# Performance work log

Hardware: AMD Instinct MI355X
Metric: run time of the kernel (lower is better)

The kernel has to match this reference:

```python
import jax, jax.numpy as jnp
import numpy as np

N, C, H, W = 8, 80, 100, 152          # batch, fg classes, stride-8 feature map of 800x1216 image
STRIDE = 8
P = H * W                              # points in this level
PRE_NMS_THRESH = 0.05                  # cfg.post.INFERENCE_TH
PRE_NMS_TOP_N = 1000                   # cfg.post.PRE_NMS_TOP_N
NMS_THRESH = 0.6                       # cfg.post.NMS_TH
POST_NMS_TOP_N = 100                   # cfg.post.DETECTIONS_PER_IMG
MIN_SIZE = 0.0
CLASS_OFFSET = 1.0e5                   # per-class NMS via coordinate-offset trick


def setup_inputs():
    key = jax.random.key(0)
    k1, k2, k3 = jax.random.split(key, 3)
    ys, xs = jnp.meshgrid(jnp.arange(H), jnp.arange(W), indexing='ij')
    locations = (jnp.stack([xs.reshape(-1), ys.reshape(-1)], axis=1).astype(jnp.float32) * STRIDE + STRIDE // 2)
    box_cls = jax.random.normal(k1, (N, C, H, W), jnp.float32) - 2.0
    box_regression = jax.random.uniform(k2, (N, 4, H, W), jnp.float32) * 64.0
    centerness = jax.random.normal(k3, (N, 1, H, W), jnp.float32)
    im_info = jnp.tile(jnp.array([[H * STRIDE, W * STRIDE]], jnp.float32), (N, 1))
    return {'locations': locations, 'box_cls': box_cls, 'box_regression': box_regression,
            'centerness': centerness, 'im_info': im_info}


def _iou_matrix(boxes):
    # boxes: [K, 4] (x1, y1, x2, y2)
    area = jnp.clip(boxes[:, 2] - boxes[:, 0], 0) * jnp.clip(boxes[:, 3] - boxes[:, 1], 0)
    lt = jnp.maximum(boxes[:, None, :2], boxes[None, :, :2])
    rb = jnp.minimum(boxes[:, None, 2:], boxes[None, :, 2:])
    wh = jnp.clip(rb - lt, 0)
    inter = wh[..., 0] * wh[..., 1]
    return inter / (area[:, None] + area[None, :] - inter + 1e-9)


def _single_image(locations, cls_logits, reg, ctr_logits, info):
    # [C,H,W] -> [P,C] matches permute(0,2,3,1).reshape(-1,C)
    cls = jax.nn.sigmoid(cls_logits.reshape(C, P).T)
    ctr = jax.nn.sigmoid(ctr_logits.reshape(P))
    cand = cls > PRE_NMS_THRESH
    scores = cls * ctr[:, None]
    flat = jnp.where(cand, scores, 0.0).reshape(-1)          # [P*C], zeros = non-candidates
    topv, topi = jax.lax.top_k(flat, PRE_NMS_TOP_N)          # pre-NMS top-n (sorted desc)
    loc = topi // C
    label = topi % C + 1
    valid = topv > 0.0
    r = reg.reshape(4, P).T[loc]                             # [K, 4] (l, t, r, b)
    pt = locations[loc]                                      # [K, 2]
    h_im, w_im = info[0], info[1]
    x1 = jnp.clip(pt[:, 0] - r[:, 0], 0.0, w_im - 1.0)
    y1 = jnp.clip(pt[:, 1] - r[:, 1], 0.0, h_im - 1.0)
    x2 = jnp.clip(pt[:, 0] + r[:, 2], 0.0, w_im - 1.0)
    y2 = jnp.clip(pt[:, 1] + r[:, 3], 0.0, h_im - 1.0)
    boxes = jnp.stack([x1, y1, x2, y2], axis=1)
    valid = valid & (x2 - x1 >= MIN_SIZE) & (y2 - y1 >= MIN_SIZE)  # remove_small_boxes
    sc = jnp.where(valid, topv, 0.0)
    # offset boxes by class so cross-class IoU is 0 -> equivalent to per-class NMS
    ob = boxes + (label.astype(boxes.dtype) * CLASS_OFFSET)[:, None]
    iou = _iou_matrix(ob)
    idx = jnp.arange(PRE_NMS_TOP_N)
    def body(i, keep):
        alive = keep[i] & valid[i]
        sup = alive & (iou[i] > NMS_THRESH) & (idx > i)
        return keep & ~sup
    keep = jax.lax.fori_loop(0, PRE_NMS_TOP_N, body, valid)  # greedy NMS (score-sorted)
    final_sc = jnp.where(keep, sc, 0.0)
    fv, fi = jax.lax.top_k(final_sc, POST_NMS_TOP_N)         # detections-per-image cap
    out = jnp.concatenate([boxes[fi], label[fi][:, None].astype(boxes.dtype), fv[:, None]], axis=1)
    return jnp.where((fv > 0.0)[:, None], out, 0.0)          # [POST_NMS_TOP_N, 6]


def reference(locations, box_cls, box_regression, centerness, im_info):
    # -> [N, POST_NMS_TOP_N, 6] = (x1, y1, x2, y2, label, score), zero-padded rows invalid
    return jax.vmap(lambda c, r, t, i: _single_image(locations, c, r, t, i))(
        box_cls, box_regression, centerness, im_info)
```

## Files before the change

### kernel.cpp

```cpp
#include <hip/hip_runtime.h>
#include <stdint.h>

#define NIMG 8
#define NCLS 80
#define HF 100
#define WF 152
#define NPTS (HF*WF)
#define NPC (NPTS*NCLS)
#define NF4 (NPC/4)
#define TOPK 1000
#define NSH 8
#define SHCAP 512
#define SORTN 4096
#define LBUF 1024
#define POSTK 100
#define HBLK 297
#define RBLK (SORTN/256)

static constexpr size_t B_H1    = 0;
static constexpr size_t B_CNT   = B_H1 + (size_t)NIMG*4096*4;
static constexpr size_t B_META  = B_CNT + (size_t)NIMG*NSH*4;
static constexpr size_t B_BMAX  = B_META + NIMG*4*4;
static constexpr size_t B_SKEY  = (B_BMAX + (size_t)NIMG*HBLK*4 + 7) & ~(size_t)7;
static constexpr size_t B_ZEND  = B_SKEY + (size_t)NIMG*1024*8;
static constexpr size_t B_CTRS  = (B_ZEND + 15) & ~(size_t)15;
static constexpr size_t B_CAND  = (B_CTRS + (size_t)NIMG*NPTS*4 + 15) & ~(size_t)15;
static constexpr size_t B_BOX   = B_CAND + (size_t)NIMG*NSH*SHCAP*8;
static constexpr size_t B_OBOX  = B_BOX + (size_t)NIMG*TOPK*16;
static constexpr size_t B_SC    = B_OBOX + (size_t)NIMG*TOPK*16;
static constexpr size_t B_VAL   = B_SC + (size_t)NIMG*TOPK*4;
static constexpr size_t B_LAB   = B_VAL + (size_t)NIMG*TOPK*4;
static constexpr size_t B_KEEP  = B_LAB + (size_t)NIMG*TOPK*4;

__device__ __forceinline__ float sigm(float x){ return 1.0f / (1.0f + expf(-x)); }

__global__ void __launch_bounds__(256)
k_ctrsig(const float* __restrict__ ctr, float* __restrict__ ctr_sig){
  int i4 = blockIdx.x * 256 + threadIdx.x;
  if (i4 < NIMG*NPTS/4){
    float4 v = ((const float4*)ctr)[i4];
    float4 o;
    o.x = sigm(v.x); o.y = sigm(v.y); o.z = sigm(v.z); o.w = sigm(v.w);
    ((float4*)ctr_sig)[i4] = o;
  }
}

__global__ void __launch_bounds__(256)
k_hist(const float* __restrict__ box_cls, const float* __restrict__ ctr_sig,
       uint32_t* __restrict__ h1, uint32_t* __restrict__ bmax){
  __shared__ uint32_t h[4096];
  __shared__ uint32_t smax;
  for (int i = threadIdx.x; i < 4096; i += 256) h[i] = 0;
  if (threadIdx.x == 0) smax = 0;
  __syncthreads();
  const int n = blockIdx.y;
  const float4* cls4 = (const float4*)(box_cls + (size_t)n * NPC);
  const float* cs = ctr_sig + (size_t)n * NPTS;
  const int base4 = blockIdx.x * 1024 + threadIdx.x;
  float4 a[4], b[4];
  bool ok[4];
  #pragma unroll
  for (int k = 0; k < 4; ++k){
    int i4 = base4 + k * 256;
    ok[k] = (i4 < NF4);
    if (ok[k]){
      a[k] = cls4[i4];
      uint32_t p0 = ((uint32_t)(i4 << 2)) % (uint32_t)NPTS;
      b[k] = *(const float4*)(cs + p0);
    }
  }
  __builtin_amdgcn_sched_barrier(0);
  uint32_t vmax = 0;
  #pragma unroll
  for (int k = 0; k < 4; ++k){
    if (!ok[k]) continue;
    float sv[4] = {a[k].x, a[k].y, a[k].z, a[k].w};
    float cv[4] = {b[k].x, b[k].y, b[k].z, b[k].w};
    #pragma unroll
    for (int j = 0; j < 4; ++j){
      float s = sigm(sv[j]);
      if (s > 0.05f){
        float sc = s * cv[j];
        if (sc > 0.0f){
          uint32_t bin = __float_as_uint(sc) >> 18;
          atomicAdd(&h[bin], 1u);
          vmax = (bin > vmax) ? bin : vmax;
        }
      }
    }
  }
  if (vmax) atomicMax(&smax, vmax);
  __syncthreads();
  uint32_t* g = h1 + (size_t)n * 4096;
  for (int i = threadIdx.x; i < 4096; i += 256){
    uint32_t v = h[i];
    if (v) atomicAdd(&g[i], v);
  }
  if (threadIdx.x == 0) bmax[n * HBLK + blockIdx.x] = smax;
}

__global__ void k_scan(const uint32_t* __restrict__ h1, uint32_t* __restrict__ meta){
  const int n = blockIdx.x;
  const uint32_t* h = h1 + (size_t)n * 4096;
  __shared__ uint32_t psum[256];
  __shared__ uint32_t suff[256];
  const int t = threadIdx.x;
  uint32_t s = 0;
  #pragma unroll
  for (int i = 0; i < 16; ++i) s += h[t * 16 + i];
  psum[t] = s;
  __syncthreads();
  if (t == 0){
    uint32_t acc = 0;
    for (int seg = 255; seg >= 0; --seg){ suff[seg] = acc; acc += psum[seg]; }
  }
  __syncthreads();
  if (suff[t] < TOPK && suff[t] + psum[t] >= TOPK){
    uint32_t acc = suff[t];
    for (int b = t * 16 + 15; b >= t * 16; --b){
      uint32_t hb = h[b];
      if (acc + hb >= TOPK){
        meta[n * 4 + 0] = acc;
        meta[n * 4 + 1] = (uint32_t)b;
        break;
      }
      acc += hb;
    }
  }
}

__global__ void __launch_bounds__(256)
k_collect(const float* __restrict__ box_cls, const float* __restrict__ ctr_sig,
          const uint32_t* __restrict__ meta, const uint32_t* __restrict__ bmax,
          uint32_t* __restrict__ cnt, uint64_t* __restrict__ cand){
  __shared__ uint64_t buf[LBUF];
  __shared__ uint32_t lcnt;
  __shared__ uint32_t gbase;
  const int n = blockIdx.y;
  const uint32_t T = meta[n * 4 + 1];
  if (bmax[n * HBLK + blockIdx.x] < T) return;
  if (threadIdx.x == 0) lcnt = 0;
  __syncthreads();
  const float4* cls4 = (const float4*)(box_cls + (size_t)n * NPC);
  const float* cs = ctr_sig + (size_t)n * NPTS;
  const int base4 = blockIdx.x * 1024 + threadIdx.x;
  float4 a[4], b[4];
  int p0a[4], ca[4];
  bool ok[4];
  #pragma unroll
  for (int k = 0; k < 4; ++k){
    int i4 = base4 + k * 256;
    ok[k] = (i4 < NF4);
    if (ok[k]){
      a[k] = cls4[i4];
      uint32_t e0 = (uint32_t)(i4 << 2);
      uint32_t c = e0 / (uint32_t)NPTS;
      uint32_t p0 = e0 - c * (uint32_t)NPTS;
      ca[k] = (int)c; p0a[k] = (int)p0;
      b[k] = *(const float4*)(cs + p0);
    }
  }
  __builtin_amdgcn_sched_barrier(0);
  #pragma unroll
  for (int k = 0; k < 4; ++k){
    if (!ok[k]) continue;
    float sv[4] = {a[k].x, a[k].y, a[k].z, a[k].w};
    float cv[4] = {b[k].x, b[k].y, b[k].z, b[k].w};
    #pragma unroll
    for (int j = 0; j < 4; ++j){
      float s = sigm(sv[j]);
      if (s > 0.05f){
        float sc = s * cv[j];
        if (sc > 0.0f){
          uint32_t bits = __float_as_uint(sc);
          if ((bits >> 18) >= T){
            uint32_t f = (uint32_t)(p0a[k] + j) * NCLS + (uint32_t)ca[k];
            uint32_t pos = atomicAdd(&lcnt, 1u);
            if (pos < LBUF)
              buf[pos] = ((uint64_t)bits << 32) | (uint64_t)(0xFFFFFFFFu - f);
          }
        }
      }
    }
  }
  __syncthreads();
  uint32_t c = lcnt; if (c > LBUF) c = LBUF;
  const int sh = blockIdx.x & (NSH - 1);
  if (threadIdx.x == 0 && c) gbase = atomicAdd(&cnt[n * NSH + sh], c);
  __syncthreads();
  for (uint32_t i = threadIdx.x; i < c; i += 256){
    uint32_t p = gbase + i;
    if (p < SHCAP) cand[(((size_t)n * NSH + sh) << 9) + p] = buf[i];
  }
}

__global__ void __launch_bounds__(256)
k_rank(const uint32_t* __restrict__ cnt, const uint64_t* __restrict__ cand,
       uint64_t* __restrict__ skey){
  __shared__ alignas(16) uint64_t keys[SORTN + 4];
  __shared__ uint32_t cs_s[NSH], pre_s[NSH + 1];
  const int n = blockIdx.y;
  const int t = threadIdx.x;
  if (t == 0){
    uint32_t acc = 0;
    for (int s = 0; s < NSH; ++s){
      uint32_t c = cnt[n * NSH + s]; if (c > SHCAP) c = SHCAP;
      cs_s[s] = c; pre_s[s] = acc; acc += c;
    }
    pre_s[NSH] = acc;
  }
  __syncthreads();
  const int total = (int)pre_s[NSH];
  const int base = blockIdx.x * 256;
  if (base >= total) return;
  for (int i = t; i < SORTN; i += 256){
    int s = i >> 9, j = i & (SHCAP - 1);
    if ((uint32_t)j < cs_s[s])
      keys[pre_s[s] + j] = cand[(((size_t)n * NSH + s) << 9) + j];
  }
  if (t < 4) keys[total + t] = 0ull;
  __syncthreads();
  const int g = base + t;
  const uint64_t my = (g < total) ? keys[g] : 0ull;
  uint32_t rank = 0;
  const int tot4 = (total + 3) & ~3;
  for (int i = 0; i < tot4; i += 4){
    rank += (keys[i]     > my) ? 1u : 0u;
    rank += (keys[i + 1] > my) ? 1u : 0u;
    rank += (keys[i + 2] > my) ? 1u : 0u;
    rank += (keys[i + 3] > my) ? 1u : 0u;
  }
  if (g < total && rank < TOPK)
    skey[(size_t)n * 1024 + rank] = my;
}

__global__ void __launch_bounds__(1024)
k_decode(const uint64_t* __restrict__ skey,
         const float* __restrict__ locations, const float* __restrict__ box_reg,
         const float* __restrict__ im_info,
         float* __restrict__ boxw, float* __restrict__ oboxw, float* __restrict__ scw,
         uint32_t* __restrict__ valw, uint32_t* __restrict__ labw){
  const int n = blockIdx.x;
  const int t = threadIdx.x;
  if (t < TOPK){
    uint64_t kk = skey[(size_t)n * 1024 + t];
    uint32_t bits = (uint32_t)(kk >> 32);
    uint32_t fi = 0xFFFFFFFFu - (uint32_t)(kk & 0xFFFFFFFFull);
    float v = __uint_as_float(bits);
    int loc = 0, ci = 0;
    if (v > 0.0f){ loc = (int)(fi / NCLS); ci = (int)(fi - (uint32_t)loc * NCLS); }
    float px = locations[2 * loc], py = locations[2 * loc + 1];
    const float* rg = box_reg + (size_t)n * 4 * NPTS;
    float rl = rg[loc], rt = rg[NPTS + loc], rr = rg[2 * NPTS + loc], rb = rg[3 * NPTS + loc];
    float h_im = im_info[n * 2 + 0], w_im = im_info[n * 2 + 1];
    float x1 = fminf(fmaxf(px - rl, 0.0f), w_im - 1.0f);
    float y1 = fminf(fmaxf(py - rt, 0.0f), h_im - 1.0f);
    float x2 = fminf(fmaxf(px + rr, 0.0f), w_im - 1.0f);
    float y2 = fminf(fmaxf(py + rb, 0.0f), h_im - 1.0f);
    bool valid = (v > 0.0f) && (__fsub_rn(x2, x1) >= 0.0f) && (__fsub_rn(y2, y1) >= 0.0f);
    float scv = valid ? v : 0.0f;
    float lab = (float)(ci + 1);
    float off = __fmul_rn(lab, 100000.0f);
    size_t b4 = ((size_t)n * TOPK + t) * 4;
    boxw[b4 + 0] = x1; boxw[b4 + 1] = y1; boxw[b4 + 2] = x2; boxw[b4 + 3] = y2;
    oboxw[b4 + 0] = __fadd_rn(x1, off); oboxw[b4 + 1] = __fadd_rn(y1, off);
    oboxw[b4 + 2] = __fadd_rn(x2, off); oboxw[b4 + 3] = __fadd_rn(y2, off);
    size_t b1 = (size_t)n * TOPK + t;
    scw[b1] = scv; valw[b1] = valid ? 1u : 0u; labw[b1] = (uint32_t)(ci + 1);
  }
}

__global__ void __launch_bounds__(64)
k_nms(const uint32_t* __restrict__ labw, const float* __restrict__ oboxw,
      const uint32_t* __restrict__ valw, uint32_t* __restrict__ keepw){
  const int n = blockIdx.y;
  const int c = blockIdx.x;
  const int L = threadIdx.x;
  __shared__ uint16_t lst_s[TOPK];
  const uint32_t target = (uint32_t)(c + 1);
  uint32_t kcnt = 0;
  for (int i0 = 0; i0 < TOPK; i0 += 64){
    int slot = i0 + L;
    uint32_t lab = (slot < TOPK) ? labw[n * TOPK + slot] : 0u;
    bool m = (lab == target);
    uint64_t mask = __ballot(m);
    uint32_t pre = (uint32_t)__popcll(mask & ((1ull << L) - 1ull));
    if (m) lst_s[kcnt + pre] = (uint16_t)slot;
    kcnt += (uint32_t)__popcll(mask);
  }
  __syncthreads();
  if (kcnt == 0) return;
  if (kcnt <= 64){
    int gi = 0, kp = 0;
    float b0 = 0, b1 = 0, b2 = 0, b3 = 0, ar = 0;
    if (L < (int)kcnt){
      gi = (int)lst_s[L];
      size_t a4 = ((size_t)n * TOPK + gi) * 4;
      b0 = oboxw[a4 + 0]; b1 = oboxw[a4 + 1]; b2 = oboxw[a4 + 2]; b3 = oboxw[a4 + 3];
      kp = (valw[n * TOPK + gi] != 0) ? 1 : 0;
      ar = __fmul_rn(fmaxf(__fsub_rn(b2, b0), 0.0f), fmaxf(__fsub_rn(b3, b1), 0.0f));
    }
    for (int i = 0; i + 1 < (int)kcnt; ++i){
      int alive = __shfl(kp, i);
      float xi0 = __shfl(b0, i), xi1 = __shfl(b1, i), xi2 = __shfl(b2, i), xi3 = __shfl(b3, i);
      float ai = __shfl(ar, i);
      if (alive && L > i && kp){
        float ltx = fmaxf(xi0, b0), lty = fmaxf(xi1, b1);
        float rbx = fminf(xi2, b2), rby = fminf(xi3, b3);
        float w = fmaxf(__fsub_rn(rbx, ltx), 0.0f);
        float h = fmaxf(__fsub_rn(rby, lty), 0.0f);
        float inter = __fmul_rn(w, h);
        float den = __fadd_rn(__fsub_rn(__fadd_rn(ai, ar), inter), 1e-9f);
        if (inter / den > 0.6f) kp = 0;
      }
    }
    if (L < (int)kcnt) keepw[n * TOPK + gi] = (uint32_t)kp;
  } else if (L == 0){
    for (uint32_t i = 0; i < kcnt; ++i){
      int gi = (int)lst_s[i];
      keepw[n * TOPK + gi] = valw[n * TOPK + gi];
    }
    for (uint32_t i = 0; i < kcnt; ++i){
      int gi = (int)lst_s[i];
      if (!keepw[n * TOPK + gi]) continue;
      size_t a4 = ((size_t)n * TOPK + gi) * 4;
      float x0 = oboxw[a4], x1 = oboxw[a4 + 1], x2 = oboxw[a4 + 2], x3 = oboxw[a4 + 3];
      float ai = __fmul_rn(fmaxf(__fsub_rn(x2, x0), 0.0f), fmaxf(__fsub_rn(x3, x1), 0.0f));
      for (uint32_t j = i + 1; j < kcnt; ++j){
        int gj = (int)lst_s[j];
        if (!keepw[n * TOPK + gj]) continue;
        size_t c4 = ((size_t)n * TOPK + gj) * 4;
        float y0 = oboxw[c4], y1 = oboxw[c4 + 1], y2 = oboxw[c4 + 2], y3 = oboxw[c4 + 3];
        float aj = __fmul_rn(fmaxf(__fsub_rn(y2, y0), 0.0f), fmaxf(__fsub_rn(y3, y1), 0.0f));
        float ltx = fmaxf(x0, y0), lty = fmaxf(x1, y1);
        float rbx = fminf(x2, y2), rby = fminf(x3, y3);
        float w = fmaxf(__fsub_rn(rbx, ltx), 0.0f);
        float h = fmaxf(__fsub_rn(rby, lty), 0.0f);
        float inter = __fmul_rn(w, h);
        float den = __fadd_rn(__fsub_rn(__fadd_rn(ai, aj), inter), 1e-9f);
        if (inter / den > 0.6f) keepw[n * TOPK + gj] = 0;
      }
    }
  }
}

__global__ void __launch_bounds__(256)
k_final(const uint32_t* __restrict__ keepw, const float* __restrict__ boxw,
        const uint32_t* __restrict__ labw, const float* __restrict__ scw,
        float* __restrict__ out){
  const int n = blockIdx.x;
  __shared__ uint16_t fi_s[TOPK];
  __shared__ uint32_t wsum[4];
  const int t = threadIdx.x;
  const int i0 = t * 4;
  uint32_t f[4];
  #pragma unroll
  for (int j = 0; j < 4; ++j)
    f[j] = (i0 + j < TOPK) ? keepw[n * TOPK + i0 + j] : 0u;
  uint32_t lsum = f[0] + f[1] + f[2] + f[3];
  uint32_t sc = lsum;
  #pragma unroll
  for (int d = 1; d < 64; d <<= 1){
    uint32_t v = __shfl_up(sc, d);
    if ((t & 63) >= d) sc += v;
  }
  if ((t & 63) == 63) wsum[t >> 6] = sc;
  __syncthreads();
  uint32_t base = sc - lsum;
  for (int w = 0; w < (t >> 6); ++w) base += wsum[w];
  uint32_t p = base;
  #pragma unroll
  for (int j = 0; j < 4; ++j){
    if (f[j]){ if (p < TOPK) fi_s[p] = (uint16_t)(i0 + j); ++p; }
  }
  __syncthreads();
  uint32_t total = wsum[0] + wsum[1] + wsum[2] + wsum[3];
  if (t < POSTK){
    float* row = out + ((size_t)n * POSTK + t) * 6;
    if (t < (int)total){
      int i = (int)fi_s[t];
      size_t b4 = ((size_t)n * TOPK + i) * 4;
      row[0] = boxw[b4]; row[1] = boxw[b4 + 1]; row[2] = boxw[b4 + 2]; row[3] = boxw[b4 + 3];
      row[4] = (float)labw[n * TOPK + i]; row[5] = scw[n * TOPK + i];
    } else {
      row[0] = 0.0f; row[1] = 0.0f; row[2] = 0.0f;
      row[3] = 0.0f; row[4] = 0.0f; row[5] = 0.0f;
    }
  }
}

extern "C" void kernel_launch(void* const* d_in, const int* in_sizes, int n_in,
                              void* d_out, int out_size, void* d_ws, size_t ws_size,
                              hipStream_t stream){
  const float* locations = (const float*)d_in[0];
  const float* box_cls   = (const float*)d_in[1];
  const float* box_reg   = (const float*)d_in[2];
  const float* ctr       = (const float*)d_in[3];
  const float* im_info   = (const float*)d_in[4];
  float* out = (float*)d_out;
  char* ws = (char*)d_ws;
  uint32_t* h1    = (uint32_t*)(ws + B_H1);
  uint32_t* cnt   = (uint32_t*)(ws + B_CNT);
  uint32_t* meta  = (uint32_t*)(ws + B_META);
  uint32_t* bmax  = (uint32_t*)(ws + B_BMAX);
  uint64_t* skey  = (uint64_t*)(ws + B_SKEY);
  float*    ctrs  = (float*)(ws + B_CTRS);
  uint64_t* cand  = (uint64_t*)(ws + B_CAND);
  float*    boxw  = (float*)(ws + B_BOX);
  float*    oboxw = (float*)(ws + B_OBOX);
  float*    scw   = (float*)(ws + B_SC);
  uint32_t* valw  = (uint32_t*)(ws + B_VAL);
  uint32_t* labw  = (uint32_t*)(ws + B_LAB);
  uint32_t* keepw = (uint32_t*)(ws + B_KEEP);

  hipMemsetAsync(d_ws, 0, B_ZEND, stream);
  k_ctrsig<<<dim3((NIMG*NPTS/4 + 255)/256), 256, 0, stream>>>(ctr, ctrs);
  dim3 scang(HBLK, NIMG);
  k_hist<<<scang, 256, 0, stream>>>(box_cls, ctrs, h1, bmax);
  k_scan<<<NIMG, 256, 0, stream>>>(h1, meta);
  k_collect<<<scang, 256, 0, stream>>>(box_cls, ctrs, meta, bmax, cnt, cand);
  k_rank<<<dim3(RBLK, NIMG), 256, 0, stream>>>(cnt, cand, skey);
  k_decode<<<NIMG, 1024, 0, stream>>>(skey, locations, box_reg, im_info,
                                      boxw, oboxw, scw, valw, labw);
  k_nms<<<dim3(NCLS, NIMG), 64, 0, stream>>>(labw, oboxw, valw, keepw);
  k_final<<<NIMG, 256, 0, stream>>>(keepw, boxw, labw, scw, out);
}
```

Before: 190.5 us.

## Fuse decode, NMS and final compaction into one LDS-resident tail kernel

Merges the decode, per-class NMS and final compaction kernels into a single kernel per image. Boxes, scores, labels and keep flags stay in shared memory, and 16 wavefronts each handle a subset of classes. It also drops the workspace hipMemsetAsync by having the centerness-sigmoid kernel zero the histogram, counter and key buffers. The aim is to cut launch overhead and global round-trips. In exchange, per-class NMS runs on 16 waves per image instead of 80 independent blocks, so there is less parallelism in that phase.

```diff
diff --git a/kernel.cpp b/kernel.cpp
--- a/kernel.cpp
+++ b/kernel.cpp
@@ -16,33 +16,31 @@
 #define POSTK 100
 #define HBLK 297
 #define RBLK (SORTN/256)
-
-static constexpr size_t B_H1    = 0;
-static constexpr size_t B_CNT   = B_H1 + (size_t)NIMG*4096*4;
-static constexpr size_t B_META  = B_CNT + (size_t)NIMG*NSH*4;
-static constexpr size_t B_BMAX  = B_META + NIMG*4*4;
-static constexpr size_t B_SKEY  = (B_BMAX + (size_t)NIMG*HBLK*4 + 7) & ~(size_t)7;
-static constexpr size_t B_ZEND  = B_SKEY + (size_t)NIMG*1024*8;
-static constexpr size_t B_CTRS  = (B_ZEND + 15) & ~(size_t)15;
-static constexpr size_t B_CAND  = (B_CTRS + (size_t)NIMG*NPTS*4 + 15) & ~(size_t)15;
-static constexpr size_t B_BOX   = B_CAND + (size_t)NIMG*NSH*SHCAP*8;
-static constexpr size_t B_OBOX  = B_BOX + (size_t)NIMG*TOPK*16;
-static constexpr size_t B_SC    = B_OBOX + (size_t)NIMG*TOPK*16;
-static constexpr size_t B_VAL   = B_SC + (size_t)NIMG*TOPK*4;
-static constexpr size_t B_LAB   = B_VAL + (size_t)NIMG*TOPK*4;
-static constexpr size_t B_KEEP  = B_LAB + (size_t)NIMG*TOPK*4;
+#define ZWORDS (NIMG*4096 + NIMG*NSH + NIMG*4)
+
+static constexpr size_t B_H1   = 0;
+static constexpr size_t B_CNT  = B_H1 + (size_t)NIMG*4096*4;
+static constexpr size_t B_META = B_CNT + (size_t)NIMG*NSH*4;
+static constexpr size_t B_BMAX = B_META + NIMG*4*4;
+static constexpr size_t B_SKEY = (B_BMAX + (size_t)NIMG*HBLK*4 + 7) & ~(size_t)7;
+static constexpr size_t B_CTRS = (B_SKEY + (size_t)NIMG*1024*8 + 15) & ~(size_t)15;
+static constexpr size_t B_CAND = (B_CTRS + (size_t)NIMG*NPTS*4 + 15) & ~(size_t)15;
 
 __device__ __forceinline__ float sigm(float x){ return 1.0f / (1.0f + expf(-x)); }
 
 __global__ void __launch_bounds__(256)
-k_ctrsig(const float* __restrict__ ctr, float* __restrict__ ctr_sig){
-  int i4 = blockIdx.x * 256 + threadIdx.x;
-  if (i4 < NIMG*NPTS/4){
-    float4 v = ((const float4*)ctr)[i4];
+k_ctrsig(const float* __restrict__ ctr, float* __restrict__ ctr_sig,
+         uint32_t* __restrict__ zr, uint64_t* __restrict__ skey){
+  const int gid = blockIdx.x * 256 + threadIdx.x;
+  const int nthr = 119 * 256;
+  if (gid < NIMG*NPTS/4){
+    float4 v = ((const float4*)ctr)[gid];
     float4 o;
     o.x = sigm(v.x); o.y = sigm(v.y); o.z = sigm(v.z); o.w = sigm(v.w);
-    ((float4*)ctr_sig)[i4] = o;
-  }
+    ((float4*)ctr_sig)[gid] = o;
+  }
+  for (int i = gid; i < ZWORDS; i += nthr) zr[i] = 0u;
+  for (int i = gid; i < NIMG*1024; i += nthr) skey[i] = 0ull;
 }
 
 __global__ void __launch_bounds__(256)
@@ -235,20 +233,28 @@
 }
 
 __global__ void __launch_bounds__(1024)
-k_decode(const uint64_t* __restrict__ skey,
-         const float* __restrict__ locations, const float* __restrict__ box_reg,
-         const float* __restrict__ im_info,
-         float* __restrict__ boxw, float* __restrict__ oboxw, float* __restrict__ scw,
-         uint32_t* __restrict__ valw, uint32_t* __restrict__ labw){
+k_tail(const uint64_t* __restrict__ skey, const float* __restrict__ locations,
+       const float* __restrict__ box_reg, const float* __restrict__ im_info,
+       float* __restrict__ out){
+  __shared__ float bx[TOPK * 4];
+  __shared__ float ob[TOPK * 4];
+  __shared__ float scs[TOPK];
+  __shared__ alignas(4) uint8_t labs[TOPK];
+  __shared__ alignas(4) uint8_t keep[TOPK];
+  __shared__ uint16_t lst[16][64];
+  __shared__ uint16_t fi[POSTK];
+  __shared__ uint32_t wsum[16];
+  __shared__ uint32_t total_s;
   const int n = blockIdx.x;
   const int t = threadIdx.x;
+  const int w = t >> 6, lane = t & 63;
   if (t < TOPK){
     uint64_t kk = skey[(size_t)n * 1024 + t];
-    uint32_t bits = (uint32_t)(kk >> 32);
-    uint32_t fi = 0xFFFFFFFFu - (uint32_t)(kk & 0xFFFFFFFFull);
-    float v = __uint_as_float(bits);
+    uint32_t bitsv = (uint32_t)(kk >> 32);
+    uint32_t fidx = 0xFFFFFFFFu - (uint32_t)(kk & 0xFFFFFFFFull);
+    float v = __uint_as_float(bitsv);
     int loc = 0, ci = 0;
-    if (v > 0.0f){ loc = (int)(fi / NCLS); ci = (int)(fi - (uint32_t)loc * NCLS); }
+    if (v > 0.0f){ loc = (int)(fidx / NCLS); ci = (int)(fidx - (uint32_t)loc * NCLS); }
     float px = locations[2 * loc], py = locations[2 * loc + 1];
     const float* rg = box_reg + (size_t)n * 4 * NPTS;
     float rl = rg[loc], rt = rg[NPTS + loc], rr = rg[2 * NPTS + loc], rb = rg[3 * NPTS + loc];
@@ -258,130 +264,89 @@
     float x2 = fminf(fmaxf(px + rr, 0.0f), w_im - 1.0f);
     float y2 = fminf(fmaxf(py + rb, 0.0f), h_im - 1.0f);
     bool valid = (v > 0.0f) && (__fsub_rn(x2, x1) >= 0.0f) && (__fsub_rn(y2, y1) >= 0.0f);
-    float scv = valid ? v : 0.0f;
-    float lab = (float)(ci + 1);
-    float off = __fmul_rn(lab, 100000.0f);
-    size_t b4 = ((size_t)n * TOPK + t) * 4;
-    boxw[b4 + 0] = x1; boxw[b4 + 1] = y1; boxw[b4 + 2] = x2; boxw[b4 + 3] = y2;
-    oboxw[b4 + 0] = __fadd_rn(x1, off); oboxw[b4 + 1] = __fadd_rn(y1, off);
-    oboxw[b4 + 2] = __fadd_rn(x2, off); oboxw[b4 + 3] = __fadd_rn(y2, off);
-    size_t b1 = (size_t)n * TOPK + t;
-    scw[b1] = scv; valw[b1] = valid ? 1u : 0u; labw[b1] = (uint32_t)(ci + 1);
-  }
-}
-
-__global__ void __launch_bounds__(64)
-k_nms(const uint32_t* __restrict__ labw, const float* __restrict__ oboxw,
-      const uint32_t* __restrict__ valw, uint32_t* __restrict__ keepw){
-  const int n = blockIdx.y;
-  const int c = blockIdx.x;
-  const int L = threadIdx.x;
-  __shared__ uint16_t lst_s[TOPK];
-  const uint32_t target = (uint32_t)(c + 1);
-  uint32_t kcnt = 0;
-  for (int i0 = 0; i0 < TOPK; i0 += 64){
-    int slot = i0 + L;
-    uint32_t lab = (slot < TOPK) ? labw[n * TOPK + slot] : 0u;
-    bool m = (lab == target);
-    uint64_t mask = __ballot(m);
-    uint32_t pre = (uint32_t)__popcll(mask & ((1ull << L) - 1ull));
-    if (m) lst_s[kcnt + pre] = (uint16_t)slot;
-    kcnt += (uint32_t)__popcll(mask);
-  }
-  __syncthreads();
-  if (kcnt == 0) return;
-  if (kcnt <= 64){
-    int gi = 0, kp = 0;
-    float b0 = 0, b1 = 0, b2 = 0, b3 = 0, ar = 0;
-    if (L < (int)kcnt){
-      gi = (int)lst_s[L];
-      size_t a4 = ((size_t)n * TOPK + gi) * 4;
-      b0 = oboxw[a4 + 0]; b1 = oboxw[a4 + 1]; b2 = oboxw[a4 + 2]; b3 = oboxw[a4 + 3];
-      kp = (valw[n * TOPK + gi] != 0) ? 1 : 0;
-      ar = __fmul_rn(fmaxf(__fsub_rn(b2, b0), 0.0f), fmaxf(__fsub_rn(b3, b1), 0.0f));
-    }
-    for (int i = 0; i + 1 < (int)kcnt; ++i){
-      int alive = __shfl(kp, i);
-      float xi0 = __shfl(b0, i), xi1 = __shfl(b1, i), xi2 = __shfl(b2, i), xi3 = __shfl(b3, i);
-      float ai = __shfl(ar, i);
-      if (alive && L > i && kp){
-        float ltx = fmaxf(xi0, b0), lty = fmaxf(xi1, b1);
-        float rbx = fminf(xi2, b2), rby = fminf(xi3, b3);
-        float w = fmaxf(__fsub_rn(rbx, ltx), 0.0f);
-        float h = fmaxf(__fsub_rn(rby, lty), 0.0f);
-        float inter = __fmul_rn(w, h);
-        float den = __fadd_rn(__fsub_rn(__fadd_rn(ai, ar), inter), 1e-9f);
-        if (inter / den > 0.6f) kp = 0;
-      }
-    }
-    if (L < (int)kcnt) keepw[n * TOPK + gi] = (uint32_t)kp;
-  } else if (L == 0){
-    for (uint32_t i = 0; i < kcnt; ++i){
-      int gi = (int)lst_s[i];
-      keepw[n * TOPK + gi] = valw[n * TOPK + gi];
-    }
-    for (uint32_t i = 0; i < kcnt; ++i){
-      int gi = (int)lst_s[i];
-      if (!keepw[n * TOPK + gi]) continue;
-      size_t a4 = ((size_t)n * TOPK + gi) * 4;
-      float x0 = oboxw[a4], x1 = oboxw[a4 + 1], x2 = oboxw[a4 + 2], x3 = oboxw[a4 + 3];
-      float ai = __fmul_rn(fmaxf(__fsub_rn(x2, x0), 0.0f), fmaxf(__fsub_rn(x3, x1), 0.0f));
-      for (uint32_t j = i + 1; j < kcnt; ++j){
-        int gj = (int)lst_s[j];
-        if (!keepw[n * TOPK + gj]) continue;
-        size_t c4 = ((size_t)n * TOPK + gj) * 4;
-        float y0 = oboxw[c4], y1 = oboxw[c4 + 1], y2 = oboxw[c4 + 2], y3 = oboxw[c4 + 3];
-        float aj = __fmul_rn(fmaxf(__fsub_rn(y2, y0), 0.0f), fmaxf(__fsub_rn(y3, y1), 0.0f));
-        float ltx = fmaxf(x0, y0), lty = fmaxf(x1, y1);
-        float rbx = fminf(x2, y2), rby = fminf(x3, y3);
-        float w = fmaxf(__fsub_rn(rbx, ltx), 0.0f);
-        float h = fmaxf(__fsub_rn(rby, lty), 0.0f);
-        float inter = __fmul_rn(w, h);
-        float den = __fadd_rn(__fsub_rn(__fadd_rn(ai, aj), inter), 1e-9f);
-        if (inter / den > 0.6f) keepw[n * TOPK + gj] = 0;
-      }
-    }
-  }
-}
-
-__global__ void __launch_bounds__(256)
-k_final(const uint32_t* __restrict__ keepw, const float* __restrict__ boxw,
-        const uint32_t* __restrict__ labw, const float* __restrict__ scw,
-        float* __restrict__ out){
-  const int n = blockIdx.x;
-  __shared__ uint16_t fi_s[TOPK];
-  __shared__ uint32_t wsum[4];
-  const int t = threadIdx.x;
-  const int i0 = t * 4;
-  uint32_t f[4];
-  #pragma unroll
-  for (int j = 0; j < 4; ++j)
-    f[j] = (i0 + j < TOPK) ? keepw[n * TOPK + i0 + j] : 0u;
-  uint32_t lsum = f[0] + f[1] + f[2] + f[3];
-  uint32_t sc = lsum;
-  #pragma unroll
-  for (int d = 1; d < 64; d <<= 1){
-    uint32_t v = __shfl_up(sc, d);
-    if ((t & 63) >= d) sc += v;
-  }
-  if ((t & 63) == 63) wsum[t >> 6] = sc;
-  __syncthreads();
-  uint32_t base = sc - lsum;
-  for (int w = 0; w < (t >> 6); ++w) base += wsum[w];
-  uint32_t p = base;
-  #pragma unroll
-  for (int j = 0; j < 4; ++j){
-    if (f[j]){ if (p < TOPK) fi_s[p] = (uint16_t)(i0 + j); ++p; }
-  }
-  __syncthreads();
-  uint32_t total = wsum[0] + wsum[1] + wsum[2] + wsum[3];
+    float off = __fmul_rn((float)(ci + 1), 100000.0f);
+    bx[t*4+0] = x1; bx[t*4+1] = y1; bx[t*4+2] = x2; bx[t*4+3] = y2;
+    ob[t*4+0] = __fadd_rn(x1, off); ob[t*4+1] = __fadd_rn(y1, off);
+    ob[t*4+2] = __fadd_rn(x2, off); ob[t*4+3] = __fadd_rn(y2, off);
+    scs[t] = valid ? v : 0.0f;
+    labs[t] = (uint8_t)ci;
+    keep[t] = valid ? 1 : 0;
+  }
+  __syncthreads();
+  for (int ci = w; ci < NCLS; ci += 16){
+    uint32_t kcnt = 0;
+    for (int i0 = 0; i0 < TOPK; i0 += 64){
+      int slot = i0 + lane;
+      bool m = (slot < TOPK) && (labs[slot] == (uint8_t)ci);
+      uint64_t mask = __ballot(m);
+      uint32_t pre = (uint32_t)__popcll(mask & ((1ull << lane) - 1ull));
+      uint32_t idx = kcnt + pre;
+      if (m && idx < 64) lst[w][idx] = (uint16_t)slot;
+      kcnt += (uint32_t)__popcll(mask);
+    }
+    if (kcnt == 0) continue;
+    if (kcnt <= 64){
+      int gi = 0, kp = 0;
+      float b0 = 0, b1 = 0, b2 = 0, b3 = 0, ar = 0;
+      if (lane < (int)kcnt){
+        gi = (int)lst[w][lane];
+        b0 = ob[gi*4+0]; b1 = ob[gi*4+1]; b2 = ob[gi*4+2]; b3 = ob[gi*4+3];
+        kp = keep[gi];
+        ar = __fmul_rn(fmaxf(__fsub_rn(b2, b0), 0.0f), fmaxf(__fsub_rn(b3, b1), 0.0f));
+      }
+      for (int i = 0; i + 1 < (int)kcnt; ++i){
+        int alive = __shfl(kp, i);
+        float xi0 = __shfl(b0, i), xi1 = __shfl(b1, i), xi2 = __shfl(b2, i), xi3 = __shfl(b3, i);
+        float ai = __shfl(ar, i);
+        if (alive && lane > i && kp){
+          float ltx = fmaxf(xi0, b0), lty = fmaxf(xi1, b1);
+          float rbx = fminf(xi2, b2), rby = fminf(xi3, b3);
+          float ww = fmaxf(__fsub_rn(rbx, ltx), 0.0f);
+          float hh = fmaxf(__fsub_rn(rby, lty), 0.0f);
+          float inter = __fmul_rn(ww, hh);
+          float den = __fadd_rn(__fsub_rn(__fadd_rn(ai, ar), inter), 1e-9f);
+          if (inter / den > 0.6f) kp = 0;
+        }
+      }
+      if (lane < (int)kcnt) keep[gi] = (uint8_t)kp;
+    } else if (lane == 0){
+      for (int i = 0; i < TOPK; ++i){
+        if (labs[i] != (uint8_t)ci || !keep[i]) continue;
+        float x0 = ob[i*4], x1 = ob[i*4+1], x2 = ob[i*4+2], x3 = ob[i*4+3];
+        float ai = __fmul_rn(fmaxf(__fsub_rn(x2, x0), 0.0f), fmaxf(__fsub_rn(x3, x1), 0.0f));
+        for (int jj = i + 1; jj < TOPK; ++jj){
+          if (labs[jj] != (uint8_t)ci || !keep[jj]) continue;
+          float y0 = ob[jj*4], y1 = ob[jj*4+1], y2 = ob[jj*4+2], y3 = ob[jj*4+3];
+          float aj = __fmul_rn(fmaxf(__fsub_rn(y2, y0), 0.0f), fmaxf(__fsub_rn(y3, y1), 0.0f));
+          float ltx = fmaxf(x0, y0), lty = fmaxf(x1, y1);
+          float rbx = fminf(x2, y2), rby = fminf(x3, y3);
+          float ww = fmaxf(__fsub_rn(rbx, ltx), 0.0f);
+          float hh = fmaxf(__fsub_rn(rby, lty), 0.0f);
+          float inter = __fmul_rn(ww, hh);
+          float den = __fadd_rn(__fsub_rn(__fadd_rn(ai, aj), inter), 1e-9f);
+          if (inter / den > 0.6f) keep[jj] = 0;
+        }
+      }
+    }
+  }
+  __syncthreads();
+  uint32_t kp = (t < TOPK) ? (uint32_t)keep[t] : 0u;
+  uint64_t mask = __ballot(kp != 0u);
+  uint32_t pre = (uint32_t)__popcll(mask & ((1ull << lane) - 1ull));
+  if (lane == 0) wsum[w] = (uint32_t)__popcll(mask);
+  __syncthreads();
+  uint32_t base = 0;
+  for (int i = 0; i < w; ++i) base += wsum[i];
+  uint32_t p = base + pre;
+  if (kp && p < POSTK) fi[p] = (uint16_t)t;
+  if (t == 0){ uint32_t tt = 0; for (int i = 0; i < 16; ++i) tt += wsum[i]; total_s = tt; }
+  __syncthreads();
   if (t < POSTK){
     float* row = out + ((size_t)n * POSTK + t) * 6;
-    if (t < (int)total){
-      int i = (int)fi_s[t];
-      size_t b4 = ((size_t)n * TOPK + i) * 4;
-      row[0] = boxw[b4]; row[1] = boxw[b4 + 1]; row[2] = boxw[b4 + 2]; row[3] = boxw[b4 + 3];
-      row[4] = (float)labw[n * TOPK + i]; row[5] = scw[n * TOPK + i];
+    if (t < (int)total_s){
+      int i = (int)fi[t];
+      row[0] = bx[i*4]; row[1] = bx[i*4+1]; row[2] = bx[i*4+2]; row[3] = bx[i*4+3];
+      row[4] = (float)(labs[i] + 1); row[5] = scs[i];
     } else {
       row[0] = 0.0f; row[1] = 0.0f; row[2] = 0.0f;
       row[3] = 0.0f; row[4] = 0.0f; row[5] = 0.0f;
@@ -399,29 +364,19 @@
   const float* im_info   = (const float*)d_in[4];
   float* out = (float*)d_out;
   char* ws = (char*)d_ws;
-  uint32_t* h1    = (uint32_t*)(ws + B_H1);
-  uint32_t* cnt   = (uint32_t*)(ws + B_CNT);
-  uint32_t* meta  = (uint32_t*)(ws + B_META);
-  uint32_t* bmax  = (uint32_t*)(ws + B_BMAX);
-  uint64_t* skey  = (uint64_t*)(ws + B_SKEY);
-  float*    ctrs  = (float*)(ws + B_CTRS);
-  uint64_t* cand  = (uint64_t*)(ws + B_CAND);
-  float*    boxw  = (float*)(ws + B_BOX);
-  float*    oboxw = (float*)(ws + B_OBOX);
-  float*    scw   = (float*)(ws + B_SC);
-  uint32_t* valw  = (uint32_t*)(ws + B_VAL);
-  uint32_t* labw  = (uint32_t*)(ws + B_LAB);
-  uint32_t* keepw = (uint32_t*)(ws + B_KEEP);
-
-  hipMemsetAsync(d_ws, 0, B_ZEND, stream);
-  k_ctrsig<<<dim3((NIMG*NPTS/4 + 255)/256), 256, 0, stream>>>(ctr, ctrs);
+  uint32_t* h1   = (uint32_t*)(ws + B_H1);
+  uint32_t* cnt  = (uint32_t*)(ws + B_CNT);
+  uint32_t* meta = (uint32_t*)(ws + B_META);
+  uint32_t* bmax = (uint32_t*)(ws + B_BMAX);
+  uint64_t* skey = (uint64_t*)(ws + B_SKEY);
+  float*    ctrs = (float*)(ws + B_CTRS);
+  uint64_t* cand = (uint64_t*)(ws + B_CAND);
+
+  k_ctrsig<<<dim3(119), 256, 0, stream>>>(ctr, ctrs, h1, skey);
   dim3 scang(HBLK, NIMG);
   k_hist<<<scang, 256, 0, stream>>>(box_cls, ctrs, h1, bmax);
   k_scan<<<NIMG, 256, 0, stream>>>(h1, meta);
   k_collect<<<scang, 256, 0, stream>>>(box_cls, ctrs, meta, bmax, cnt, cand);
   k_rank<<<dim3(RBLK, NIMG), 256, 0, stream>>>(cnt, cand, skey);
-  k_decode<<<NIMG, 1024, 0, stream>>>(skey, locations, box_reg, im_info,
-                                      boxw, oboxw, scw, valw, labw);
-  k_nms<<<dim3(NCLS, NIMG), 64, 0, stream>>>(labw, oboxw, valw, keepw);
-  k_final<<<NIMG, 256, 0, stream>>>(keepw, boxw, labw, scw, out);
-}
+  k_tail<<<NIMG, 1024, 0, stream>>>(skey, locations, box_reg, im_info, out);
+}
```

Measured after the change: 200.3 us. 5.1% more time.

## Replace full-pass histogram threshold with sampled threshold plus exact fallback

Applied to the files above, without the earlier changes.

Replaces the full histogram pass over all class scores with a per-image sample of 32 strided float4 chunks, used to estimate a conservative score threshold for candidate collection. This removes one full read of box_cls along with the global histogram and scan kernels. Zeroing moves into the centerness sigmoid kernel, so the memset is dropped. A per-image fallback kernel redoes an exact histogram and collection when the sampled threshold yields too few or too many candidates, which adds a launch and slow serial work when the sample misjudges the threshold.

```diff
diff --git a/kernel.cpp b/kernel.cpp
--- a/kernel.cpp
+++ b/kernel.cpp
@@ -16,95 +16,76 @@
 #define POSTK 100
 #define HBLK 297
 #define RBLK (SORTN/256)
-
-static constexpr size_t B_H1    = 0;
-static constexpr size_t B_CNT   = B_H1 + (size_t)NIMG*4096*4;
-static constexpr size_t B_META  = B_CNT + (size_t)NIMG*NSH*4;
-static constexpr size_t B_BMAX  = B_META + NIMG*4*4;
-static constexpr size_t B_SKEY  = (B_BMAX + (size_t)NIMG*HBLK*4 + 7) & ~(size_t)7;
-static constexpr size_t B_ZEND  = B_SKEY + (size_t)NIMG*1024*8;
-static constexpr size_t B_CTRS  = (B_ZEND + 15) & ~(size_t)15;
-static constexpr size_t B_CAND  = (B_CTRS + (size_t)NIMG*NPTS*4 + 15) & ~(size_t)15;
-static constexpr size_t B_BOX   = B_CAND + (size_t)NIMG*NSH*SHCAP*8;
-static constexpr size_t B_OBOX  = B_BOX + (size_t)NIMG*TOPK*16;
-static constexpr size_t B_SC    = B_OBOX + (size_t)NIMG*TOPK*16;
-static constexpr size_t B_VAL   = B_SC + (size_t)NIMG*TOPK*4;
-static constexpr size_t B_LAB   = B_VAL + (size_t)NIMG*TOPK*4;
-static constexpr size_t B_KEEP  = B_LAB + (size_t)NIMG*TOPK*4;
+#define SCHUNK 32
+#define SSTRIDE 9500
+#define SM_T 65
+
+static constexpr size_t B_CNT  = 0;
+static constexpr size_t B_META = B_CNT + (size_t)NIMG*NSH*4;
+static constexpr size_t B_SKEY = (B_META + NIMG*4*4 + 7) & ~(size_t)7;
+static constexpr size_t B_CTRS = (B_SKEY + (size_t)NIMG*1024*8 + 15) & ~(size_t)15;
+static constexpr size_t B_CAND = (B_CTRS + (size_t)NIMG*NPTS*4 + 15) & ~(size_t)15;
+static constexpr size_t B_BOX  = B_CAND + (size_t)NIMG*NSH*SHCAP*8;
+static constexpr size_t B_OBOX = B_BOX + (size_t)NIMG*TOPK*16;
+static constexpr size_t B_SC   = B_OBOX + (size_t)NIMG*TOPK*16;
+static constexpr size_t B_VAL  = B_SC + (size_t)NIMG*TOPK*4;
+static constexpr size_t B_LAB  = B_VAL + (size_t)NIMG*TOPK*4;
+static constexpr size_t B_KEEP = B_LAB + (size_t)NIMG*TOPK*4;
+#define ZWORDS (NIMG*NSH + NIMG*4)
 
 __device__ __forceinline__ float sigm(float x){ return 1.0f / (1.0f + expf(-x)); }
 
 __global__ void __launch_bounds__(256)
-k_ctrsig(const float* __restrict__ ctr, float* __restrict__ ctr_sig){
-  int i4 = blockIdx.x * 256 + threadIdx.x;
-  if (i4 < NIMG*NPTS/4){
-    float4 v = ((const float4*)ctr)[i4];
+k_ctrsig(const float* __restrict__ ctr, float* __restrict__ ctr_sig,
+         uint32_t* __restrict__ zr, uint64_t* __restrict__ skey){
+  const int gid = blockIdx.x * 256 + threadIdx.x;
+  const int nthr = 119 * 256;
+  if (gid < NIMG*NPTS/4){
+    float4 v = ((const float4*)ctr)[gid];
     float4 o;
     o.x = sigm(v.x); o.y = sigm(v.y); o.z = sigm(v.z); o.w = sigm(v.w);
-    ((float4*)ctr_sig)[i4] = o;
-  }
+    ((float4*)ctr_sig)[gid] = o;
+  }
+  for (int i = gid; i < ZWORDS; i += nthr) zr[i] = 0u;
+  for (int i = gid; i < NIMG*1024; i += nthr) skey[i] = 0ull;
 }
 
 __global__ void __launch_bounds__(256)
-k_hist(const float* __restrict__ box_cls, const float* __restrict__ ctr_sig,
-       uint32_t* __restrict__ h1, uint32_t* __restrict__ bmax){
+k_sample(const float* __restrict__ box_cls, const float* __restrict__ ctr_sig,
+         uint32_t* __restrict__ meta){
   __shared__ uint32_t h[4096];
-  __shared__ uint32_t smax;
-  for (int i = threadIdx.x; i < 4096; i += 256) h[i] = 0;
-  if (threadIdx.x == 0) smax = 0;
-  __syncthreads();
-  const int n = blockIdx.y;
+  __shared__ uint32_t psum[256], suff[256];
+  const int n = blockIdx.x;
+  const int t = threadIdx.x;
+  for (int i = t; i < 4096; i += 256) h[i] = 0;
+  __syncthreads();
   const float4* cls4 = (const float4*)(box_cls + (size_t)n * NPC);
   const float* cs = ctr_sig + (size_t)n * NPTS;
-  const int base4 = blockIdx.x * 1024 + threadIdx.x;
-  float4 a[4], b[4];
-  bool ok[4];
-  #pragma unroll
-  for (int k = 0; k < 4; ++k){
-    int i4 = base4 + k * 256;
-    ok[k] = (i4 < NF4);
-    if (ok[k]){
-      a[k] = cls4[i4];
-      uint32_t p0 = ((uint32_t)(i4 << 2)) % (uint32_t)NPTS;
+  for (int c0 = 0; c0 < SCHUNK; c0 += 4){
+    float4 a[4], b[4];
+    #pragma unroll
+    for (int k = 0; k < 4; ++k){
+      int g = (c0 + k) * SSTRIDE + t;
+      a[k] = cls4[g];
+      uint32_t p0 = ((uint32_t)(g << 2)) % (uint32_t)NPTS;
       b[k] = *(const float4*)(cs + p0);
     }
-  }
-  __builtin_amdgcn_sched_barrier(0);
-  uint32_t vmax = 0;
-  #pragma unroll
-  for (int k = 0; k < 4; ++k){
-    if (!ok[k]) continue;
-    float sv[4] = {a[k].x, a[k].y, a[k].z, a[k].w};
-    float cv[4] = {b[k].x, b[k].y, b[k].z, b[k].w};
+    __builtin_amdgcn_sched_barrier(0);
     #pragma unroll
-    for (int j = 0; j < 4; ++j){
-      float s = sigm(sv[j]);
-      if (s > 0.05f){
-        float sc = s * cv[j];
-        if (sc > 0.0f){
-          uint32_t bin = __float_as_uint(sc) >> 18;
-          atomicAdd(&h[bin], 1u);
-          vmax = (bin > vmax) ? bin : vmax;
+    for (int k = 0; k < 4; ++k){
+      float sv[4] = {a[k].x, a[k].y, a[k].z, a[k].w};
+      float cv[4] = {b[k].x, b[k].y, b[k].z, b[k].w};
+      #pragma unroll
+      for (int j = 0; j < 4; ++j){
+        float s = sigm(sv[j]);
+        if (s > 0.05f){
+          float sc = s * cv[j];
+          if (sc > 0.0f) atomicAdd(&h[__float_as_uint(sc) >> 18], 1u);
         }
       }
     }
   }
-  if (vmax) atomicMax(&smax, vmax);
-  __syncthreads();
-  uint32_t* g = h1 + (size_t)n * 4096;
-  for (int i = threadIdx.x; i < 4096; i += 256){
-    uint32_t v = h[i];
-    if (v) atomicAdd(&g[i], v);
-  }
-  if (threadIdx.x == 0) bmax[n * HBLK + blockIdx.x] = smax;
-}
-
-__global__ void k_scan(const uint32_t* __restrict__ h1, uint32_t* __restrict__ meta){
-  const int n = blockIdx.x;
-  const uint32_t* h = h1 + (size_t)n * 4096;
-  __shared__ uint32_t psum[256];
-  __shared__ uint32_t suff[256];
-  const int t = threadIdx.x;
+  __syncthreads();
   uint32_t s = 0;
   #pragma unroll
   for (int i = 0; i < 16; ++i) s += h[t * 16 + i];
@@ -115,13 +96,12 @@
     for (int seg = 255; seg >= 0; --seg){ suff[seg] = acc; acc += psum[seg]; }
   }
   __syncthreads();
-  if (suff[t] < TOPK && suff[t] + psum[t] >= TOPK){
+  if (suff[t] < SM_T && suff[t] + psum[t] >= SM_T){
     uint32_t acc = suff[t];
     for (int b = t * 16 + 15; b >= t * 16; --b){
       uint32_t hb = h[b];
-      if (acc + hb >= TOPK){
-        meta[n * 4 + 0] = acc;
-        meta[n * 4 + 1] = (uint32_t)b;
+      if (acc + hb >= SM_T){
+        meta[n * 4 + 1] = ((uint32_t)b) << 18;
         break;
       }
       acc += hb;
@@ -130,15 +110,14 @@
 }
 
 __global__ void __launch_bounds__(256)
-k_collect(const float* __restrict__ box_cls, const float* __restrict__ ctr_sig,
-          const uint32_t* __restrict__ meta, const uint32_t* __restrict__ bmax,
-          uint32_t* __restrict__ cnt, uint64_t* __restrict__ cand){
+k_main(const float* __restrict__ box_cls, const float* __restrict__ ctr_sig,
+       const uint32_t* __restrict__ meta,
+       uint32_t* __restrict__ cnt, uint64_t* __restrict__ cand){
   __shared__ uint64_t buf[LBUF];
   __shared__ uint32_t lcnt;
   __shared__ uint32_t gbase;
   const int n = blockIdx.y;
-  const uint32_t T = meta[n * 4 + 1];
-  if (bmax[n * HBLK + blockIdx.x] < T) return;
+  const uint32_t Traw = meta[n * 4 + 1];
   if (threadIdx.x == 0) lcnt = 0;
   __syncthreads();
   const float4* cls4 = (const float4*)(box_cls + (size_t)n * NPC);
@@ -173,7 +152,7 @@
         float sc = s * cv[j];
         if (sc > 0.0f){
           uint32_t bits = __float_as_uint(sc);
-          if ((bits >> 18) >= T){
+          if (bits >= Traw){
             uint32_t f = (uint32_t)(p0a[k] + j) * NCLS + (uint32_t)ca[k];
             uint32_t pos = atomicAdd(&lcnt, 1u);
             if (pos < LBUF)
@@ -191,6 +170,88 @@
   for (uint32_t i = threadIdx.x; i < c; i += 256){
     uint32_t p = gbase + i;
     if (p < SHCAP) cand[(((size_t)n * NSH + sh) << 9) + p] = buf[i];
+  }
+}
+
+__global__ void __launch_bounds__(1024)
+k_fallback(const float* __restrict__ box_cls, const float* __restrict__ ctr_sig,
+           const uint32_t* __restrict__ meta,
+           uint32_t* __restrict__ cnt, uint64_t* __restrict__ cand){
+  __shared__ uint32_t h[4096];
+  __shared__ uint32_t psum[256], suff[256];
+  __shared__ uint32_t ok_s, T14_s, ctr_s;
+  const int n = blockIdx.x;
+  const int t = threadIdx.x;
+  if (t == 0){
+    uint32_t total = 0, bad = 0;
+    for (int s = 0; s < NSH; ++s){
+      uint32_t c = cnt[n * NSH + s];
+      total += c; bad |= (c > SHCAP) ? 1u : 0u;
+    }
+    uint32_t Traw = meta[n * 4 + 1];
+    ok_s = (!bad && (total >= TOPK || Traw == 0u)) ? 1u : 0u;
+    T14_s = 0; ctr_s = 0;
+  }
+  __syncthreads();
+  if (ok_s) return;
+  for (int i = t; i < 4096; i += 1024) h[i] = 0;
+  __syncthreads();
+  const float* cls = box_cls + (size_t)n * NPC;
+  const float* cs = ctr_sig + (size_t)n * NPTS;
+  for (int e = t; e < NPC; e += 1024){
+    int c = e / NPTS, p = e - c * NPTS;
+    float s = sigm(cls[e]);
+    if (s > 0.05f){
+      float sc = s * cs[p];
+      if (sc > 0.0f) atomicAdd(&h[__float_as_uint(sc) >> 18], 1u);
+    }
+  }
+  __syncthreads();
+  if (t < 256){
+    uint32_t s = 0;
+    #pragma unroll
+    for (int i = 0; i < 16; ++i) s += h[t * 16 + i];
+    psum[t] = s;
+  }
+  __syncthreads();
+  if (t == 0){
+    uint32_t acc = 0;
+    for (int seg = 255; seg >= 0; --seg){ suff[seg] = acc; acc += psum[seg]; }
+  }
+  __syncthreads();
+  if (t < 256 && suff[t] < TOPK && suff[t] + psum[t] >= TOPK){
+    uint32_t acc = suff[t];
+    for (int b = t * 16 + 15; b >= t * 16; --b){
+      uint32_t hb = h[b];
+      if (acc + hb >= TOPK){ T14_s = (uint32_t)b; break; }
+      acc += hb;
+    }
+  }
+  __syncthreads();
+  const uint32_t Traw2 = T14_s << 18;
+  if (t < NSH) cnt[n * NSH + t] = 0;
+  __syncthreads();
+  for (int e = t; e < NPC; e += 1024){
+    int c = e / NPTS, p = e - c * NPTS;
+    float s = sigm(cls[e]);
+    if (s > 0.05f){
+      float sc = s * cs[p];
+      if (sc > 0.0f){
+        uint32_t bits = __float_as_uint(sc);
+        if (bits >= Traw2){
+          uint32_t f = (uint32_t)p * NCLS + (uint32_t)c;
+          uint32_t pos = atomicAdd(&ctr_s, 1u);
+          if (pos < SORTN)
+            cand[((size_t)n * NSH << 9) + pos] = ((uint64_t)bits << 32) | (uint64_t)(0xFFFFFFFFu - f);
+        }
+      }
+    }
+  }
+  __syncthreads();
+  if (t < NSH){
+    uint32_t total = ctr_s; if (total > SORTN) total = SORTN;
+    int lo = t * SHCAP;
+    cnt[n * NSH + t] = ((int)total > lo) ? ((total - lo > SHCAP) ? SHCAP : total - lo) : 0u;
   }
 }
 
@@ -399,13 +460,11 @@
   const float* im_info   = (const float*)d_in[4];
   float* out = (float*)d_out;
   char* ws = (char*)d_ws;
-  uint32_t* h1    = (uint32_t*)(ws + B_H1);
-  uint32_t* cnt   = (uint32_t*)(ws + B_CNT);
-  uint32_t* meta  = (uint32_t*)(ws + B_META);
-  uint32_t* bmax  = (uint32_t*)(ws + B_BMAX);
-  uint64_t* skey  = (uint64_t*)(ws + B_SKEY);
-  float*    ctrs  = (float*)(ws + B_CTRS);
-  uint64_t* cand  = (uint64_t*)(ws + B_CAND);
+  uint32_t* cnt  = (uint32_t*)(ws + B_CNT);
+  uint32_t* meta = (uint32_t*)(ws + B_META);
+  uint64_t* skey = (uint64_t*)(ws + B_SKEY);
+  float*    ctrs = (float*)(ws + B_CTRS);
+  uint64_t* cand = (uint64_t*)(ws + B_CAND);
   float*    boxw  = (float*)(ws + B_BOX);
   float*    oboxw = (float*)(ws + B_OBOX);
   float*    scw   = (float*)(ws + B_SC);
@@ -413,12 +472,10 @@
   uint32_t* labw  = (uint32_t*)(ws + B_LAB);
   uint32_t* keepw = (uint32_t*)(ws + B_KEEP);
 
-  hipMemsetAsync(d_ws, 0, B_ZEND, stream);
-  k_ctrsig<<<dim3((NIMG*NPTS/4 + 255)/256), 256, 0, stream>>>(ctr, ctrs);
-  dim3 scang(HBLK, NIMG);
-  k_hist<<<scang, 256, 0, stream>>>(box_cls, ctrs, h1, bmax);
-  k_scan<<<NIMG, 256, 0, stream>>>(h1, meta);
-  k_collect<<<scang, 256, 0, stream>>>(box_cls, ctrs, meta, bmax, cnt, cand);
+  k_ctrsig<<<dim3(119), 256, 0, stream>>>(ctr, ctrs, cnt, skey);
+  k_sample<<<dim3(NIMG), 256, 0, stream>>>(box_cls, ctrs, meta);
+  k_main<<<dim3(HBLK, NIMG), 256, 0, stream>>>(box_cls, ctrs, meta, cnt, cand);
+  k_fallback<<<dim3(NIMG), 1024, 0, stream>>>(box_cls, ctrs, meta, cnt, cand);
   k_rank<<<dim3(RBLK, NIMG), 256, 0, stream>>>(cnt, cand, skey);
   k_decode<<<NIMG, 1024, 0, stream>>>(skey, locations, box_reg, im_info,
                                       boxw, oboxw, scw, valw, labw);
```

After: 207.3 us. 8.8% more time.
